# Kernel tuning notes

Measured on AMD Instinct MI355X. Metric: run time of the kernel, lower is better.

The kernel has to match this reference:

```python
import jax, jax.numpy as jnp
from jax import lax
import numpy as np

N, C, T, V, M = 128, 3, 300, 25, 2
EPS = 1e-5
FLAT = 64 * 38 * 4  # 9728, encoder flatten size


def _lrelu(x):
    return jax.nn.leaky_relu(x, 0.01)


def _bn2d(x, g, b):
    # eval-mode BatchNorm2d with running_mean=0, running_var=1 (fresh init state)
    s = g * np.float32(1.0 / np.sqrt(1.0 + EPS))
    return x * s[None, :, None, None] + b[None, :, None, None]


def _conv(x, w, b):
    # Conv2d(k=3, stride=2, pad=1)
    y = lax.conv_general_dilated(x, w, (2, 2), [(1, 1), (1, 1)],
                                 dimension_numbers=('NCHW', 'OIHW', 'NCHW'))
    return y + b[None, :, None, None]


def _convT(x, w, b, out_pad):
    # ConvTranspose2d(k=3, stride=2, pad=1, output_padding=out_pad); w is torch (Cin,Cout,kh,kw)
    wt = jnp.flip(w, (2, 3)).transpose(1, 0, 2, 3)  # (Cout, Cin, kh, kw)
    pads = [(1, 1 + out_pad[0]), (1, 1 + out_pad[1])]  # k-1-pad = 1
    y = lax.conv_general_dilated(x, wt, (1, 1), pads, lhs_dilation=(2, 2),
                                 dimension_numbers=('NCHW', 'OIHW', 'NCHW'))
    return y + b[None, :, None, None]


def setup_inputs():
    key = jax.random.key(0)
    ks = iter(jax.random.split(key, 40))

    def w(shape, fan_in):
        return jax.random.normal(next(ks), shape, jnp.float32) * np.float32(1.0 / np.sqrt(fan_in))

    inp = {}
    inp['x'] = jax.random.normal(next(ks), (N, C, T, V, M), jnp.float32)
    inp['dbn_g'] = jnp.ones((150,), jnp.float32)
    inp['dbn_b'] = jnp.zeros((150,), jnp.float32)
    inp['c1_w'] = w((16, 3, 3, 3), 27)
    inp['c1_b'] = jnp.zeros((16,), jnp.float32)
    inp['bn1_g'] = jnp.ones((16,), jnp.float32)
    inp['bn1_b'] = jnp.zeros((16,), jnp.float32)
    inp['c2_w'] = w((32, 16, 3, 3), 144)
    inp['c2_b'] = jnp.zeros((32,), jnp.float32)
    inp['bn2_g'] = jnp.ones((32,), jnp.float32)
    inp['bn2_b'] = jnp.zeros((32,), jnp.float32)
    inp['c3_w'] = w((64, 32, 3, 3), 288)
    inp['c3_b'] = jnp.zeros((64,), jnp.float32)
    inp['bn3_g'] = jnp.ones((64,), jnp.float32)
    inp['bn3_b'] = jnp.zeros((64,), jnp.float32)
    inp['fc1_w'] = w((1024, FLAT), FLAT)
    inp['fc1_b'] = jnp.zeros((1024,), jnp.float32)
    inp['fc2_w'] = w((128, 1024), 1024)
    inp['fc2_b'] = jnp.zeros((128,), jnp.float32)
    inp['fc3_w'] = w((1024, 128), 128)
    inp['fc3_b'] = jnp.zeros((1024,), jnp.float32)
    inp['fc4_w'] = w((FLAT, 1024), 1024)
    inp['fc4_b'] = jnp.zeros((FLAT,), jnp.float32)
    inp['ct1_w'] = w((64, 32, 3, 3), 576)
    inp['ct1_b'] = jnp.zeros((32,), jnp.float32)
    inp['bn4_g'] = jnp.ones((32,), jnp.float32)
    inp['bn4_b'] = jnp.zeros((32,), jnp.float32)
    inp['ct2_w'] = w((32, 16, 3, 3), 288)
    inp['ct2_b'] = jnp.zeros((16,), jnp.float32)
    inp['bn5_g'] = jnp.ones((16,), jnp.float32)
    inp['bn5_b'] = jnp.zeros((16,), jnp.float32)
    inp['ct3_w'] = w((16, 3, 3, 3), 144)
    inp['ct3_b'] = jnp.zeros((3,), jnp.float32)
    return inp


def reference(x, dbn_g, dbn_b, c1_w, c1_b, bn1_g, bn1_b, c2_w, c2_b, bn2_g, bn2_b,
              c3_w, c3_b, bn3_g, bn3_b, fc1_w, fc1_b, fc2_w, fc2_b, fc3_w, fc3_b,
              fc4_w, fc4_b, ct1_w, ct1_b, bn4_g, bn4_b, ct2_w, ct2_b, bn5_g, bn5_b,
              ct3_w, ct3_b):
    n, c, t, v, m = x.shape
    # data_bn over (N, M*V*C, T), eval-mode with running_mean=0, running_var=1
    xb = x.transpose(0, 4, 3, 1, 2).reshape(n, m * v * c, t)
    s = dbn_g * np.float32(1.0 / np.sqrt(1.0 + EPS))
    xb = xb * s[None, :, None] + dbn_b[None, :, None]
    xm = xb.reshape(n, m, v, c, t).transpose(0, 1, 3, 4, 2).reshape(n * m, c, t, v)

    dm = xm[:, :, 1:, :] - xm[:, :, :-1, :]  # (NM, C, T-1, V) frame-wise motion

    # encoder
    h = _lrelu(_bn2d(_conv(dm, c1_w, c1_b), bn1_g, bn1_b))
    h = _lrelu(_bn2d(_conv(h, c2_w, c2_b), bn2_g, bn2_b))
    h = _lrelu(_bn2d(_conv(h, c3_w, c3_b), bn3_g, bn3_b))
    h = h.reshape(n * m, -1)  # (NM, 9728)
    h = _lrelu(h @ fc1_w.T + fc1_b)
    h = _lrelu(h @ fc2_w.T + fc2_b)

    # decoder
    h = _lrelu(h @ fc3_w.T + fc3_b)
    h = _lrelu(h @ fc4_w.T + fc4_b)
    h = h.reshape(n * m, 64, 38, 4)
    h = _lrelu(_bn2d(_convT(h, ct1_w, ct1_b, (1, 1)), bn4_g, bn4_b))
    h = _lrelu(_bn2d(_convT(h, ct2_w, ct2_b, (1, 1)), bn5_g, bn5_b))
    dec = jnp.tanh(_convT(h, ct3_w, ct3_b, (0, 1)))  # (NM, 3, 303, 32)

    d = dec[:, :c, :t, :v]
    d = d.at[:, :, 0, :].set(xm[:, :, 0, :])  # seed frame 0 with input positions

    # cumulative-sum-with-reset over time: the torch double loop is a scan
    z = jnp.all(dm == 0, axis=(1, 3))                       # (NM, T-1) reset flags
    z = jnp.concatenate([z, jnp.zeros((n * m, 1), bool)], 1)  # last frame never reset
    dT = d.transpose(2, 0, 1, 3)  # (T, NM, C, V)
    zT = z.T                      # (T, NM)

    def step(carry, inp):
        dt, zt = inp
        fin = jnp.where(zt[:, None, None], jnp.float32(0.0), dt + carry)
        return fin, fin

    _, outs = lax.scan(step, jnp.zeros_like(dT[0]), (dT, zT))
    r = outs.transpose(1, 2, 0, 3)  # (NM, C, T, V)
    return r.reshape(n, m, c, t, v).transpose(0, 2, 3, 4, 1)  # (N, C, T, V, M)
```

## Files before the change

### kernel.cpp

```cpp
#include <hip/hip_runtime.h>
#include <math.h>

#define LRELU(y) ((y) > 0.f ? (y) : 0.01f * (y))
__device__ __constant__ float BNS = 0.99999500003749969f;

typedef unsigned short u16;
typedef __attribute__((ext_vector_type(8))) short bf16x8;
typedef __attribute__((ext_vector_type(4))) float f32x4;

__device__ inline u16 f2b(float f) {
  union { float f; unsigned u; } x; x.f = f;
  return (u16)((x.u + 0x7FFFu + ((x.u >> 16) & 1u)) >> 16);
}
__device__ inline float b2f(u16 b) {
  union { unsigned u; float f; } x; x.u = ((unsigned)b) << 16;
  return x.f;
}
__device__ inline float4 b2f4(ushort4 u) {
  float4 r;
  r.x = b2f(u.x); r.y = b2f(u.y); r.z = b2f(u.z); r.w = b2f(u.w);
  return r;
}
__device__ inline float ldv(const float* p) { return *p; }
__device__ inline float ldv(const u16* p) { return b2f(*p); }

__device__ inline float ftanh(float x) {
  float e = __expf(2.0f * fabsf(x));
  float t = 1.0f - 2.0f / (e + 1.0f);
  return x < 0.f ? -t : t;
}

#define FM16(I0, I1, I2, I3, WV)                                        \
  a00 += (I0) * (WV).x; a01 += (I0) * (WV).y;                           \
  a02 += (I0) * (WV).z; a03 += (I0) * (WV).w;                           \
  a10 += (I1) * (WV).x; a11 += (I1) * (WV).y;                           \
  a12 += (I1) * (WV).z; a13 += (I1) * (WV).w;                           \
  a20 += (I2) * (WV).x; a21 += (I2) * (WV).y;                           \
  a22 += (I2) * (WV).z; a23 += (I2) * (WV).w;                           \
  a30 += (I3) * (WV).x; a31 += (I3) * (WV).y;                           \
  a32 += (I3) * (WV).z; a33 += (I3) * (WV).w;

#define FM12(I0, I1, I2, I3, WV)                                        \
  a0x += (I0) * (WV).x; a0y += (I0) * (WV).y; a0z += (I0) * (WV).z;     \
  a1x += (I1) * (WV).x; a1y += (I1) * (WV).y; a1z += (I1) * (WV).z;     \
  a2x += (I2) * (WV).x; a2y += (I2) * (WV).y; a2z += (I2) * (WV).z;     \
  a3x += (I3) * (WV).x; a3y += (I3) * (WV).y; a3z += (I3) * (WV).z;

__device__ __constant__ short SCH76[4][2][3] = {
  {{3, 0, 64}, {0, 0, 64}},
  {{3, 64, 76}, {0, 64, 76}},
  {{1, 0, 64}, {2, 0, 64}},
  {{1, 64, 76}, {2, 64, 76}},
};
__device__ __constant__ short SCH152[4][3][3] = {
  {{3, 0, 64}, {1, 128, 152}, {0, 0, 64}},
  {{3, 64, 128}, {2, 0, 64}, {0, 64, 128}},
  {{3, 128, 152}, {2, 64, 128}, {0, 128, 152}},
  {{1, 0, 64}, {1, 64, 128}, {2, 128, 152}},
};

__global__ __launch_bounds__(256) void cast_kernel(
    const float* __restrict__ s, u16* __restrict__ d, int n4) {
  int i = blockIdx.x * 256 + threadIdx.x;
  if (i >= n4) return;
  float4 v = ((const float4*)s)[i];
  ushort4 o;
  o.x = f2b(v.x); o.y = f2b(v.y); o.z = f2b(v.z); o.w = f2b(v.w);
  ((ushort4*)d)[i] = o;
}

__global__ __launch_bounds__(256) void wcast_fc1_kernel(
    const float* __restrict__ w, u16* __restrict__ wp) {
  int idx = blockIdx.x * 256 + threadIdx.x;
  if (idx >= 1024 * 9728) return;
  int n = idx / 9728, kp = idx % 9728;
  int sp = kp >> 6, oc = kp & 63;
  wp[idx] = f2b(w[(long)n * 9728 + oc * 152 + sp]);
}

__global__ __launch_bounds__(256) void wpad_kernel(
    const float* __restrict__ w, u16* __restrict__ wp, int OC, int K, int KP) {
  int idx = blockIdx.x * 256 + threadIdx.x;
  if (idx >= 64 * KP) return;
  int row = idx / KP, col = idx % KP;
  wp[idx] = (row < OC && col < K) ? f2b(w[row * K + col]) : (u16)0;
}

__global__ __launch_bounds__(256) void prep_kernel(
    const float* __restrict__ x, const float* __restrict__ g,
    const float* __restrict__ b, float* __restrict__ dm,
    float* __restrict__ x0) {
  int idx = blockIdx.x * 256 + threadIdx.x;
  if (idx >= 256 * 3 * 300 * 25) return;
  int v = idx % 25;
  int t = (idx / 25) % 300;
  int c = (idx / (25 * 300)) % 3;
  int nm = idx / (25 * 300 * 3);
  int n = nm >> 1, m = nm & 1;
  int ch = m * 75 + v * 3 + c;
  float s = g[ch] * BNS, bb = b[ch];
  long xi = (((long)(n * 3 + c) * 300 + t) * 25 + v) * 2 + m;
  float xm_t = x[xi] * s + bb;
  if (t == 0) x0[(nm * 3 + c) * 25 + v] = xm_t;
  if (t < 299) {
    float xm_t1 = x[xi + 50] * s + bb;
    dm[((nm * 3 + c) * 299 + t) * 25 + v] = xm_t1 - xm_t;
  }
}

__global__ __launch_bounds__(256) void zflag_kernel(
    const float* __restrict__ dm, unsigned char* __restrict__ z) {
  int gw = blockIdx.x * 4 + (threadIdx.x >> 6);
  if (gw >= 256 * 300) return;
  int lane = threadIdx.x & 63;
  int t = gw % 300, nm = gw / 300;
  bool nz = false;
  if (t < 299) {
    const float* base = dm + (long)nm * 3 * 299 * 25 + t * 25;
    if (lane < 75) {
      int c = lane / 25, v = lane % 25;
      nz = base[c * 299 * 25 + v] != 0.f;
    }
    int l2 = lane + 64;
    if (l2 < 75) {
      int c = l2 / 25, v = l2 % 25;
      nz = nz || (base[c * 299 * 25 + v] != 0.f);
    }
  }
  unsigned long long mask = __ballot(nz);
  if (lane == 0) z[nm * 300 + t] = (unsigned char)((t < 299) && (mask == 0ull));
}

template <typename TI, int IC, int OC, int OCB, int ACC, int H, int W, int OH,
          int OW, int TOH, int NTILE>
__global__ __launch_bounds__(256) void conv_tiled_kernel(
    const TI* __restrict__ in, const float* __restrict__ w,
    const float* __restrict__ cb, const float* __restrict__ bg,
    const float* __restrict__ bnb, u16* __restrict__ out) {
  constexpr int IHT = 2 * TOH + 1;
  constexpr int RL = W + 2;
  __shared__ float in_s[IC * IHT * RL];
  __shared__ float w_s[9 * IC * OCB];
  int bx = blockIdx.x;
  int nm = blockIdx.y;
  int tile = bx % NTILE;
  int oc0 = (bx / NTILE) * OCB;
  int oh0 = tile * TOH;
  int ih0 = 2 * oh0 - 1;
  const TI* inb = in + (long)nm * IC * H * W;
  for (int e = threadIdx.x; e < IC * IHT * RL; e += 256) {
    int c = e % RL;
    int r = (e / RL) % IHT;
    int ic = e / (RL * IHT);
    int ih = ih0 + r, iw = c - 1;
    float v = 0.f;
    if (ih >= 0 && ih < H && iw >= 0 && iw < W) v = ldv(&inb[(ic * H + ih) * W + iw]);
    in_s[e] = v;
  }
  for (int e = threadIdx.x; e < 9 * IC * OCB; e += 256) {
    int ocl = e % OCB;
    int ic = (e / OCB) % IC;
    int khw = e / (OCB * IC);
    int kh = khw / 3, kw = khw % 3;
    w_s[e] = w[(((oc0 + ocl) * IC + ic) * 3 + kh) * 3 + kw];
  }
  __syncthreads();
  constexpr int NPOS = TOH * OW;
  constexpr int NWI = NPOS * (OCB / ACC);
  for (int wi = threadIdx.x; wi < NWI; wi += 256) {
    int pos = wi % NPOS;
    int jb = (wi / NPOS) * ACC;
    int ow = pos % OW;
    int oh_l = pos / OW;
    int oh = oh0 + oh_l;
    if (oh >= OH) continue;
    float acc[ACC];
#pragma unroll
    for (int j = 0; j < ACC; ++j) acc[j] = 0.f;
    for (int kh = 0; kh < 3; ++kh) {
      int r = 2 * oh_l + kh;
      for (int kw = 0; kw < 3; ++kw) {
        int cc = 2 * ow + kw;
        const float* ip = &in_s[r * RL + cc];
        const float* wp = &w_s[(kh * 3 + kw) * IC * OCB + jb];
        for (int ic = 0; ic < IC; ++ic) {
          float a = ip[ic * IHT * RL];
#pragma unroll
          for (int j = 0; j < ACC; ++j) acc[j] += a * wp[ic * OCB + j];
        }
      }
    }
#pragma unroll
    for (int j = 0; j < ACC; ++j) {
      int oc = oc0 + jb + j;
      float y = (acc[j] + cb[oc]) * (bg[oc] * BNS) + bnb[oc];
      out[((long)nm * OC + oc) * OH * OW + oh * OW + ow] = f2b(LRELU(y));
    }
  }
}

template <int IC, int H, int W, int OWW, int K, int KP, bool NHWC>
__global__ __launch_bounds__(256) void im2col_kernel(
    const u16* __restrict__ in, u16* __restrict__ patch, int m_off,
    int spatial, int n_threads) {
  int idx = blockIdx.x * 256 + threadIdx.x;
  if (idx >= n_threads) return;
  constexpr int KP8 = KP / 8;
  int m = idx / KP8;
  int k0 = (idx % KP8) * 8;
  int gm = m_off + m;
  int nm = gm / spatial, sp = gm % spatial;
  int oh = sp / OWW, ow = sp % OWW;
  __align__(16) u16 vals[8];
#pragma unroll
  for (int j = 0; j < 8; ++j) {
    int k = k0 + j;
    u16 v = 0;
    if (k < K) {
      int ic = k / 9, tap = k % 9;
      int ih = 2 * oh + tap / 3 - 1, iw = 2 * ow + tap % 3 - 1;
      if ((unsigned)ih < (unsigned)H && (unsigned)iw < (unsigned)W)
        v = NHWC ? in[((long)nm * H * W + ih * W + iw) * IC + ic]
                 : in[((long)nm * IC + ic) * H * W + ih * W + iw];
    }
    vals[j] = v;
  }
  *(uint4*)(patch + (long)m * KP + k0) = *(uint4*)vals;
}

template <int EPI>
__global__ __launch_bounds__(256) void fc_mfma_kernel(
    const u16* __restrict__ A, const u16* __restrict__ Wt,
    const float* __restrict__ p0, const float* __restrict__ p1,
    const float* __restrict__ p2, u16* __restrict__ out,
    float* __restrict__ partial, int K, int N, int ksegLen, int nvalid) {
  __shared__ u16 As[64][72];
  __shared__ u16 Bs[64][72];
  int tid = threadIdx.x;
  int m0 = blockIdx.x * 64, n0 = blockIdx.y * 64;
  long kbase = (long)blockIdx.z * ksegLen;
  int row = tid >> 3;
  int seg = (tid & 7) * 8;
  const u16* ap0 = A + (long)(m0 + row) * K + kbase + seg;
  const u16* ap1 = A + (long)(m0 + row + 32) * K + kbase + seg;
  const u16* bp0 = Wt + (long)(n0 + row) * K + kbase + seg;
  const u16* bp1 = Wt + (long)(n0 + row + 32) * K + kbase + seg;
  uint4 ra0 = *(const uint4*)ap0;
  uint4 ra1 = *(const uint4*)ap1;
  uint4 rb0 = *(const uint4*)bp0;
  uint4 rb1 = *(const uint4*)bp1;
  int wv = tid >> 6, lane = tid & 63;
  int lr = lane & 15, q = lane >> 4;
  int mb = (wv >> 1) * 32, nb = (wv & 1) * 32;
  f32x4 acc[2][2] = {};
  for (int k0 = 0; k0 < ksegLen; k0 += 64) {
    *(uint4*)&As[row][seg] = ra0;
    *(uint4*)&As[row + 32][seg] = ra1;
    *(uint4*)&Bs[row][seg] = rb0;
    *(uint4*)&Bs[row + 32][seg] = rb1;
    __syncthreads();
    if (k0 + 64 < ksegLen) {
      ra0 = *(const uint4*)(ap0 + k0 + 64);
      ra1 = *(const uint4*)(ap1 + k0 + 64);
      rb0 = *(const uint4*)(bp0 + k0 + 64);
      rb1 = *(const uint4*)(bp1 + k0 + 64);
    }
#pragma unroll
    for (int kk = 0; kk < 64; kk += 32) {
      bf16x8 a0 = *(bf16x8*)&As[mb + lr][kk + q * 8];
      bf16x8 a1 = *(bf16x8*)&As[mb + 16 + lr][kk + q * 8];
      bf16x8 b0 = *(bf16x8*)&Bs[nb + lr][kk + q * 8];
      bf16x8 b1 = *(bf16x8*)&Bs[nb + 16 + lr][kk + q * 8];
      acc[0][0] = __builtin_amdgcn_mfma_f32_16x16x32_bf16(a0, b0, acc[0][0], 0, 0, 0);
      acc[0][1] = __builtin_amdgcn_mfma_f32_16x16x32_bf16(a0, b1, acc[0][1], 0, 0, 0);
      acc[1][0] = __builtin_amdgcn_mfma_f32_16x16x32_bf16(a1, b0, acc[1][0], 0, 0, 0);
      acc[1][1] = __builtin_amdgcn_mfma_f32_16x16x32_bf16(a1, b1, acc[1][1], 0, 0, 0);
    }
    __syncthreads();
  }
#pragma unroll
  for (int mi = 0; mi < 2; ++mi)
#pragma unroll
    for (int ni = 0; ni < 2; ++ni) {
      int col = n0 + nb + ni * 16 + lr;
      if (EPI == 2 && col >= nvalid) continue;
      float b0v = 0.f, scv = 1.f, shv = 0.f;
      if (EPI == 1) b0v = p0[col];
      if (EPI == 2) { b0v = p0[col]; scv = p1[col] * BNS; shv = p2[col]; }
#pragma unroll
      for (int r = 0; r < 4; ++r) {
        int grow = m0 + mb + mi * 16 + q * 4 + r;
        float y = acc[mi][ni][r];
        if (EPI == 0) {
          partial[((long)blockIdx.z * 256 + grow) * N + col] = y;
        } else if (EPI == 1) {
          out[(long)grow * N + col] = f2b(LRELU(y + b0v));
        } else {
          out[(long)grow * N + col] = f2b(LRELU((y + b0v) * scv + shv));
        }
      }
    }
}

__global__ __launch_bounds__(256) void fc_reduce_kernel(
    const float* __restrict__ partial, const float* __restrict__ bias,
    u16* __restrict__ out, int MN, int N, int S) {
  int i = blockIdx.x * 256 + threadIdx.x;
  if (i * 4 >= MN) return;
  float4 s = ((const float4*)partial)[i];
  for (int t = 1; t < S; ++t) {
    float4 p = ((const float4*)partial)[(long)t * (MN >> 2) + i];
    s.x += p.x; s.y += p.y; s.z += p.z; s.w += p.w;
  }
  int col = (i * 4) % N;
  float4 bv = *(const float4*)(bias + col);
  ushort4 o;
  o.x = f2b(LRELU(s.x + bv.x));
  o.y = f2b(LRELU(s.y + bv.y));
  o.z = f2b(LRELU(s.z + bv.z));
  o.w = f2b(LRELU(s.w + bv.w));
  ((ushort4*)out)[i] = o;
}

template <int IC, int OCTOT, int OCB, int IH, int IW, int TOH, int NTILEH>
__global__ __launch_bounds__(256) void convt_cls_kernel(
    const u16* __restrict__ in, const float* __restrict__ w,
    const float* __restrict__ cb, const float* __restrict__ bg,
    const float* __restrict__ bnb, u16* __restrict__ out) {
  constexpr int AA = TOH / 2;
  constexpr int IHT = AA + 1;
  constexpr int RW = IW + 4;
  constexpr int OH = 2 * IH, OW = 2 * IW;
  constexpr int BG = IW / 4;
  constexpr int OG = OCB / 4;
  constexpr int CLS = AA * BG * OG;
  static_assert(CLS == 76 || CLS == 152, "schedule table missing");
  constexpr int NSEG = (CLS == 76) ? 2 : 3;
  __shared__ __align__(16) u16 in_s[IC * IHT * RW];
  __shared__ __align__(16) u16 w_s[9 * IC * OCB];
  int nm = blockIdx.y;
  int tile = blockIdx.x % NTILEH;
  int oc0 = (blockIdx.x / NTILEH) * OCB;
  int oh0 = tile * TOH;
  int ihb = oh0 >> 1;
  const u16* inb = in + (long)nm * IC * IH * IW;
  for (int e = threadIdx.x; e < IC * IHT * RW; e += 256) {
    int cw = e % RW;
    int r = (e / RW) % IHT;
    int ic = e / (RW * IHT);
    int ih = ihb + r;
    u16 v = 0;
    if (cw < IW && ih < IH) v = inb[(ic * IH + ih) * IW + cw];
    in_s[e] = v;
  }
  for (int e = threadIdx.x; e < 9 * IC * OCB; e += 256) {
    int ocl = e % OCB;
    int ic = (e / OCB) % IC;
    int khw = e / (OCB * IC);
    w_s[e] = f2b(w[(ic * OCTOT + oc0 + ocl) * 9 + khw]);
  }
  __syncthreads();
  int wvid = threadIdx.x >> 6;
  int lane = threadIdx.x & 63;
  const short(*sch)[3] = (CLS == 76) ? SCH76[wvid] : SCH152[wvid];
#pragma unroll 1
  for (int s = 0; s < NSEG; ++s) {
    int c = sch[s][0];
    int i0 = sch[s][1], i1 = sch[s][2];
    int p = c >> 1, q = c & 1;
#pragma unroll 1
    for (int rem = i0 + lane; rem < i1; rem += 64) {
      int a = rem % AA;
      int t2 = rem / AA;
      int bgi = t2 % BG;
      int og = t2 / BG;
      int b0 = bgi * 4, oc = og * 4;
      float a00 = 0.f, a01 = 0.f, a02 = 0.f, a03 = 0.f;
      float a10 = 0.f, a11 = 0.f, a12 = 0.f, a13 = 0.f;
      float a20 = 0.f, a21 = 0.f, a22 = 0.f, a23 = 0.f;
      float a30 = 0.f, a31 = 0.f, a32 = 0.f, a33 = 0.f;
#pragma unroll 1
      for (int kh = 0; kh < 3; ++kh) {
        int th = p + 1 - kh;
        if (th & 1) continue;
        int r = a + (th >> 1);
        const u16* ib = &in_s[r * RW + b0];
        const u16* wb = &w_s[(kh * 3) * IC * OCB + oc];
        if (q == 0) {
#pragma unroll 1
          for (int ic = 0; ic < IC; ++ic) {
            float4 iv = b2f4(*(const ushort4*)(ib + ic * IHT * RW));
            float4 wv1 = b2f4(*(const ushort4*)(wb + (IC + ic) * OCB));
            FM16(iv.x, iv.y, iv.z, iv.w, wv1);
          }
        } else {
#pragma unroll 1
          for (int ic = 0; ic < IC; ++ic) {
            float4 iv = b2f4(*(const ushort4*)(ib + ic * IHT * RW));
            float x4 = b2f(ib[ic * IHT * RW + 4]);
            float4 wv2 = b2f4(*(const ushort4*)(wb + (2 * IC + ic) * OCB));
            FM16(iv.x, iv.y, iv.z, iv.w, wv2);
            float4 wv0 = b2f4(*(const ushort4*)(wb + ic * OCB));
            FM16(iv.y, iv.z, iv.w, x4, wv0);
          }
        }
      }
      int oh = oh0 + 2 * a + p;
      if (oh >= OH) continue;
      int ow0 = 2 * b0 + q;
#define CT_STJ(J, A0, A1, A2, A3)                                        \
      do {                                                               \
        int o_ = oc0 + oc + (J);                                         \
        float c_ = cb[o_], s_ = bg[o_] * BNS, h_ = bnb[o_];              \
        u16* op_ = out + ((long)(nm * OCTOT + o_) * OH + oh) * OW + ow0; \
        float y0_ = ((A0) + c_) * s_ + h_;                               \
        float y1_ = ((A1) + c_) * s_ + h_;                               \
        float y2_ = ((A2) + c_) * s_ + h_;                               \
        float y3_ = ((A3) + c_) * s_ + h_;                               \
        op_[0] = f2b(LRELU(y0_)); op_[2] = f2b(LRELU(y1_));              \
        op_[4] = f2b(LRELU(y2_)); op_[6] = f2b(LRELU(y3_));              \
      } while (0)
      CT_STJ(0, a00, a10, a20, a30);
      CT_STJ(1, a01, a11, a21, a31);
      CT_STJ(2, a02, a12, a22, a32);
      CT_STJ(3, a03, a13, a23, a33);
#undef CT_STJ
    }
  }
}

__global__ __launch_bounds__(256) void convt3_cls_kernel(
    const u16* __restrict__ in, const float* __restrict__ w,
    const float* __restrict__ cb, float* __restrict__ out) {
  constexpr int IC = 16, IH = 152, IW = 16, TOH = 76;
  constexpr int AA = 38, IHT = 39, RW = 20, BG = 4;
  constexpr int CH = TOH * 25;
  __shared__ __align__(16) u16 in_s[IC * IHT * RW];
  __shared__ float w_s[9 * IC * 4];
  __shared__ __align__(16) float out_s[3 * CH];
  int nm = blockIdx.y;
  int oh0 = blockIdx.x * TOH;
  int ihb = oh0 >> 1;
  const u16* inb = in + (long)nm * IC * IH * IW;
  for (int e = threadIdx.x; e < IC * IHT * RW; e += 256) {
    int cw = e % RW;
    int r = (e / RW) % IHT;
    int ic = e / (RW * IHT);
    int ih = ihb + r;
    u16 v = 0;
    if (cw < IW && ih < IH) v = inb[(ic * IH + ih) * IW + cw];
    in_s[e] = v;
  }
  for (int e = threadIdx.x; e < 9 * IC * 4; e += 256) {
    int ocl = e % 4;
    int ic = (e / 4) % IC;
    int khw = e / 64;
    w_s[e] = (ocl < 3) ? w[(ic * 3 + ocl) * 9 + khw] : 0.f;
  }
  __syncthreads();
  float cb0 = cb[0], cb1 = cb[1], cb2 = cb[2];
  int wvid = threadIdx.x >> 6;
  int lane = threadIdx.x & 63;
  const short(*sch)[3] = SCH152[wvid];
#pragma unroll 1
  for (int s = 0; s < 3; ++s) {
    int c = sch[s][0];
    int i0 = sch[s][1], i1 = sch[s][2];
    int p = c >> 1, q = c & 1;
#pragma unroll 1
    for (int rem = i0 + lane; rem < i1; rem += 64) {
      int a = rem % AA;
      int bgi = rem / AA;
      int b0 = bgi * 4;
      float a0x = 0.f, a0y = 0.f, a0z = 0.f;
      float a1x = 0.f, a1y = 0.f, a1z = 0.f;
      float a2x = 0.f, a2y = 0.f, a2z = 0.f;
      float a3x = 0.f, a3y = 0.f, a3z = 0.f;
#pragma unroll 1
      for (int kh = 0; kh < 3; ++kh) {
        int th = p + 1 - kh;
        if (th & 1) continue;
        int r = a + (th >> 1);
        const u16* ib = &in_s[r * RW + b0];
        const float* wb = &w_s[(kh * 3) * IC * 4];
        if (q == 0) {
#pragma unroll 1
          for (int ic = 0; ic < IC; ++ic) {
            float4 iv = b2f4(*(const ushort4*)(ib + ic * IHT * RW));
            float4 wv1 = *(const float4*)(wb + (IC + ic) * 4);
            FM12(iv.x, iv.y, iv.z, iv.w, wv1);
          }
        } else {
#pragma unroll 1
          for (int ic = 0; ic < IC; ++ic) {
            float4 iv = b2f4(*(const ushort4*)(ib + ic * IHT * RW));
            float x4 = b2f(ib[ic * IHT * RW + 4]);
            float4 wv2 = *(const float4*)(wb + (2 * IC + ic) * 4);
            FM12(iv.x, iv.y, iv.z, iv.w, wv2);
            float4 wv0 = *(const float4*)(wb + ic * 4);
            FM12(iv.y, iv.z, iv.w, x4, wv0);
          }
        }
      }
      int ohl = 2 * a + p;
      int ow0 = 2 * b0 + q;
#define CT3_STB(B, AX, AY, AZ)                                           \
      do {                                                               \
        int ow_ = ow0 + 2 * (B);                                         \
        if (ow_ < 25) {                                                  \
          out_s[ohl * 25 + ow_] = (AX) + cb0;                            \
          out_s[CH + ohl * 25 + ow_] = (AY) + cb1;                       \
          out_s[2 * CH + ohl * 25 + ow_] = (AZ) + cb2;                   \
        }                                                                \
      } while (0)
      CT3_STB(0, a0x, a0y, a0z);
      CT3_STB(1, a1x, a1y, a1z);
      CT3_STB(2, a2x, a2y, a2z);
      CT3_STB(3, a3x, a3y, a3z);
#undef CT3_STB
    }
  }
  __syncthreads();
  int rows = 300 - oh0;
  if (rows > TOH) rows = TOH;
  int cnt = rows * 25;
  int tot4 = (3 * cnt) >> 2;
  for (int e4 = threadIdx.x; e4 < tot4; e4 += 256) {
    int e = e4 << 2;
    int j = e / cnt;
    int r = e - j * cnt;
    float4 v = *(const float4*)(out_s + j * CH + r);
    v.x = ftanh(v.x); v.y = ftanh(v.y); v.z = ftanh(v.z); v.w = ftanh(v.w);
    *(float4*)(out + ((long)(nm * 3 + j) * 300 + oh0) * 25 + r) = v;
  }
}

__global__ __launch_bounds__(256) void scan_kernel(
    const float* __restrict__ dec, const float* __restrict__ x0,
    const unsigned char* __restrict__ z, float* __restrict__ out) {
  int idx = blockIdx.x * 256 + threadIdx.x;
  if (idx >= 256 * 75) return;
  int v = idx % 25;
  int c = (idx / 25) % 3;
  int nm = idx / 75;
  int n = nm >> 1, m = nm & 1;
  const float* db = dec + ((long)(nm * 3 + c) * 300) * 25 + v;
  const unsigned char* zb = z + nm * 300;
  float* ob = out + (((long)(n * 3 + c) * 300) * 25 + v) * 2 + m;
  float x0v = x0[(nm * 3 + c) * 25 + v];
  float carry = 0.f;
  for (int t0 = 0; t0 < 300; t0 += 10) {
    float vals[10];
#pragma unroll
    for (int i = 0; i < 10; ++i) vals[i] = db[(t0 + i) * 25];
#pragma unroll
    for (int i = 0; i < 10; ++i) {
      int t = t0 + i;
      float d = (t == 0) ? x0v : vals[i];
      carry = zb[t] ? 0.f : (d + carry);
      ob[(long)t * 50] = carry;
    }
  }
}

extern "C" void kernel_launch(void* const* d_in, const int* in_sizes, int n_in,
                              void* d_out, int out_size, void* d_ws, size_t ws_size,
                              hipStream_t stream) {
  const float* x     = (const float*)d_in[0];
  const float* dbn_g = (const float*)d_in[1];
  const float* dbn_b = (const float*)d_in[2];
  const float* c1_w  = (const float*)d_in[3];
  const float* c1_b  = (const float*)d_in[4];
  const float* bn1_g = (const float*)d_in[5];
  const float* bn1_b = (const float*)d_in[6];
  const float* c2_w  = (const float*)d_in[7];
  const float* c2_b  = (const float*)d_in[8];
  const float* bn2_g = (const float*)d_in[9];
  const float* bn2_b = (const float*)d_in[10];
  const float* c3_w  = (const float*)d_in[11];
  const float* c3_b  = (const float*)d_in[12];
  const float* bn3_g = (const float*)d_in[13];
  const float* bn3_b = (const float*)d_in[14];
  const float* fc1_w = (const float*)d_in[15];
  const float* fc1_b = (const float*)d_in[16];
  const float* fc2_w = (const float*)d_in[17];
  const float* fc2_b = (const float*)d_in[18];
  const float* fc3_w = (const float*)d_in[19];
  const float* fc3_b = (const float*)d_in[20];
  const float* fc4_w = (const float*)d_in[21];
  const float* fc4_b = (const float*)d_in[22];
  const float* ct1_w = (const float*)d_in[23];
  const float* ct1_b = (const float*)d_in[24];
  const float* bn4_g = (const float*)d_in[25];
  const float* bn4_b = (const float*)d_in[26];
  const float* ct2_w = (const float*)d_in[27];
  const float* ct2_b = (const float*)d_in[28];
  const float* bn5_g = (const float*)d_in[29];
  const float* bn5_b = (const float*)d_in[30];
  const float* ct3_w = (const float*)d_in[31];
  const float* ct3_b = (const float*)d_in[32];
  float* out = (float*)d_out;

  char* ws = (char*)d_ws;
  unsigned char* zbuf = (unsigned char*)ws;
  float* x0 = (float*)(ws + 131072);
  char* slotA = ws + 262144;
  float* dm   = (float*)slotA;
  u16*   wbA  = (u16*)slotA;
  float* ct3o = (float*)slotA;
  char* slotB = ws + 23461888;
  u16* c1o  = (u16*)slotB;
  u16* ct2o = (u16*)slotB;
  char* slotP = ws + 44433408;
  u16*   patch   = (u16*)slotP;
  float* partial = (float*)slotP;
  u16*   ct1o    = (u16*)slotP;
  char* slotD = ws + 70254592;
  u16* c2o = (u16*)slotD;
  u16* f4  = (u16*)slotD;
  u16* c3o = (u16*)(ws + 78954496);
  u16* wb2   = (u16*)(ws + 83968000);
  u16* wb3   = (u16*)(ws + 84230144);
  u16* f1    = (u16*)(ws + 84492288);
  u16* f2    = (u16*)(ws + 85016576);
  u16* f3    = (u16*)(ws + 85082112);
  u16* w2pad = (u16*)(ws + 85606400);
  u16* w3pad = (u16*)(ws + 85630976);

  prep_kernel<<<22500, 256, 0, stream>>>(x, dbn_g, dbn_b, dm, x0);
  zflag_kernel<<<19200, 256, 0, stream>>>(dm, zbuf);

  conv_tiled_kernel<float, 3, 16, 16, 8, 299, 25, 150, 13, 30, 5>
      <<<dim3(5, 256), 256, 0, stream>>>(dm, c1_w, c1_b, bn1_g, bn1_b, c1o);

  wcast_fc1_kernel<<<38912, 256, 0, stream>>>(fc1_w, wbA);
  cast_kernel<<<128, 256, 0, stream>>>(fc2_w, wb2, 32768);
  cast_kernel<<<128, 256, 0, stream>>>(fc3_w, wb3, 32768);
  wpad_kernel<<<48, 256, 0, stream>>>(c2_w, w2pad, 32, 144, 192);
  wpad_kernel<<<80, 256, 0, stream>>>(c3_w, w3pad, 64, 288, 320);

  for (int h = 0; h < 2; ++h) {
    im2col_kernel<16, 150, 13, 7, 144, 192, false><<<6300, 256, 0, stream>>>(
        c1o, patch, h * 67200, 525, 67200 * 24);
    fc_mfma_kernel<2><<<dim3(1050, 1, 1), 256, 0, stream>>>(
        patch, w2pad, c2_b, bn2_g, bn2_b, c2o + (long)h * 67200 * 32, nullptr,
        192, 32, 192, 32);
  }
  im2col_kernel<32, 75, 7, 4, 288, 320, true><<<6080, 256, 0, stream>>>(
      c2o, patch, 0, 152, 38912 * 40);
  fc_mfma_kernel<2><<<dim3(608, 1, 1), 256, 0, stream>>>(
      patch, w3pad, c3_b, bn3_g, bn3_b, c3o, nullptr, 320, 64, 320, 64);

  fc_mfma_kernel<0><<<dim3(4, 16, 8), 256, 0, stream>>>(
      c3o, wbA, nullptr, nullptr, nullptr, nullptr, partial, 9728, 1024, 1216, 0);
  fc_reduce_kernel<<<256, 256, 0, stream>>>(partial, fc1_b, f1, 262144, 1024, 8);
  cast_kernel<<<9728, 256, 0, stream>>>(fc4_w, wbA, 2490368);
  fc_mfma_kernel<0><<<dim3(4, 2, 16), 256, 0, stream>>>(
      f1, wb2, nullptr, nullptr, nullptr, nullptr, partial, 1024, 128, 64, 0);
  fc_reduce_kernel<<<32, 256, 0, stream>>>(partial, fc2_b, f2, 32768, 128, 16);
  fc_mfma_kernel<0><<<dim3(4, 16, 2), 256, 0, stream>>>(
      f2, wb3, nullptr, nullptr, nullptr, nullptr, partial, 128, 1024, 64, 0);
  fc_reduce_kernel<<<256, 256, 0, stream>>>(partial, fc3_b, f3, 262144, 1024, 2);
  fc_mfma_kernel<1><<<dim3(4, 152, 1), 256, 0, stream>>>(
      f3, wbA, fc4_b, nullptr, nullptr, f4, nullptr, 1024, 9728, 1024, 9728);

  convt_cls_kernel<64, 32, 16, 38, 4, 38, 2>
      <<<dim3(4, 256), 256, 0, stream>>>(f4, ct1_w, ct1_b, bn4_g, bn4_b, ct1o);
  convt_cls_kernel<32, 16, 16, 76, 8, 38, 4>
      <<<dim3(4, 256), 256, 0, stream>>>(ct1o, ct2_w, ct2_b, bn5_g, bn5_b, ct2o);
  convt3_cls_kernel<<<dim3(4, 256), 256, 0, stream>>>(ct2o, ct3_w, ct3_b, ct3o);

  scan_kernel<<<75, 256, 0, stream>>>(ct3o, x0, zbuf, out);
}
```

Baseline: 618.3 us.

## Replace first transposed conv with MFMA sub-pixel GEMM kernel

The first ConvTranspose layer (64->32 channels, 38x4 -> 76x8) moves from the scalar FMA class-scheduled kernel to a new bf16 MFMA kernel. The kernel splits the work into four output parity classes, each computed as an implicit GEMM over only its contributing taps. A new prep kernel packs the ct1 weights per class into a padded bf16 layout. This targets the scalar FMA cost of ct1, at the price of an extra weight-pack launch, padding of N from 32 to 64 that wastes half the MFMA output columns, and uneven K across classes.

```diff
diff --git a/kernel.cpp b/kernel.cpp
--- a/kernel.cpp
+++ b/kernel.cpp
@@ -46,18 +46,22 @@
   a2x += (I2) * (WV).x; a2y += (I2) * (WV).y; a2z += (I2) * (WV).z;     \
   a3x += (I3) * (WV).x; a3y += (I3) * (WV).y; a3z += (I3) * (WV).z;
 
-__device__ __constant__ short SCH76[4][2][3] = {
-  {{3, 0, 64}, {0, 0, 64}},
-  {{3, 64, 76}, {0, 64, 76}},
-  {{1, 0, 64}, {2, 0, 64}},
-  {{1, 64, 76}, {2, 64, 76}},
-};
 __device__ __constant__ short SCH152[4][3][3] = {
   {{3, 0, 64}, {1, 128, 152}, {0, 0, 64}},
   {{3, 64, 128}, {2, 0, 64}, {0, 64, 128}},
   {{3, 128, 152}, {2, 64, 128}, {0, 128, 152}},
   {{1, 0, 64}, {1, 64, 128}, {2, 128, 152}},
 };
+
+__device__ __constant__ short CT1_TAPS[9][3] = {
+  {4, 0, 0},
+  {3, 0, 1}, {5, 0, 0},
+  {1, 1, 0}, {7, 0, 0},
+  {0, 1, 1}, {2, 1, 0}, {6, 0, 1}, {8, 0, 0},
+};
+__device__ __constant__ int CT1_TAPB[4] = {0, 1, 3, 5};
+__device__ __constant__ int CT1_K[4]    = {64, 128, 128, 256};
+__device__ __constant__ int CT1_CB[4]   = {0, 4096, 12288, 20480};
 
 __global__ __launch_bounds__(256) void cast_kernel(
     const float* __restrict__ s, u16* __restrict__ d, int n4) {
@@ -84,6 +88,20 @@
   if (idx >= 64 * KP) return;
   int row = idx / KP, col = idx % KP;
   wp[idx] = (row < OC && col < K) ? f2b(w[row * K + col]) : (u16)0;
+}
+
+__global__ __launch_bounds__(256) void wct1_kernel(
+    const float* __restrict__ w, u16* __restrict__ wt) {
+  int idx = blockIdx.x * 256 + threadIdx.x;
+  if (idx >= 36864) return;
+  int c = (idx < 4096) ? 0 : (idx < 12288) ? 1 : (idx < 20480) ? 2 : 3;
+  int off = idx - CT1_CB[c];
+  int K = CT1_K[c];
+  int n = off / K;
+  int rem = off - n * K;
+  int t = rem >> 6, ic = rem & 63;
+  int khw = CT1_TAPS[CT1_TAPB[c] + t][0];
+  wt[idx] = (n < 32) ? f2b(w[(ic * 32 + n) * 9 + khw]) : (u16)0;
 }
 
 __global__ __launch_bounds__(256) void prep_kernel(
@@ -322,6 +340,79 @@
   ((ushort4*)out)[i] = o;
 }
 
+__global__ __launch_bounds__(256) void ct1_mfma_kernel(
+    const u16* __restrict__ in, const u16* __restrict__ wt,
+    const float* __restrict__ cb, const float* __restrict__ bg,
+    const float* __restrict__ bnb, u16* __restrict__ out) {
+  constexpr int ICP = 72;
+  __shared__ __align__(16) u16 in_s[153 * ICP];
+  __shared__ __align__(16) u16 Bs[64][72];
+  int cls = blockIdx.x & 3, mt = blockIdx.x >> 2;
+  int nm = blockIdx.y;
+  int m0 = mt * 64;
+  int tid = threadIdx.x;
+  const u16* inb = in + (long)nm * 9728;
+  for (int e = tid; e < 9800; e += 256) {
+    if (e < 9728) in_s[(e % 152) * ICP + e / 152] = inb[e];
+    else in_s[152 * ICP + (e - 9728)] = 0;
+  }
+  int K = CT1_K[cls], cbase = CT1_CB[cls], tb = CT1_TAPB[cls];
+  int p = cls >> 1, qc = cls & 1;
+  int row = tid >> 3, seg = (tid & 7) * 8;
+  int wv = tid >> 6, lane = tid & 63;
+  int lr = lane & 15, qq = lane >> 4;
+  int mb = (wv >> 1) * 32, nb = (wv & 1) * 32;
+  f32x4 acc[2][2] = {};
+  int nstep = K >> 6;
+  for (int st = 0; st < nstep; ++st) {
+    __syncthreads();
+    *(uint4*)&Bs[row][seg] =
+        *(const uint4*)(wt + cbase + (long)row * K + st * 64 + seg);
+    *(uint4*)&Bs[row + 32][seg] =
+        *(const uint4*)(wt + cbase + (long)(row + 32) * K + st * 64 + seg);
+    __syncthreads();
+    int sh = CT1_TAPS[tb + st][1], sw = CT1_TAPS[tb + st][2];
+    int s0, s1;
+    {
+      int m = m0 + mb + lr;
+      int a = m >> 2, b = m & 3;
+      int ih = a + sh, iw = b + sw;
+      s0 = (m < 152 && ih < 38 && iw < 4) ? (ih * 4 + iw) : 152;
+      m = m0 + mb + 16 + lr;
+      a = m >> 2; b = m & 3; ih = a + sh; iw = b + sw;
+      s1 = (m < 152 && ih < 38 && iw < 4) ? (ih * 4 + iw) : 152;
+    }
+#pragma unroll
+    for (int kk = 0; kk < 64; kk += 32) {
+      bf16x8 a0 = *(bf16x8*)&in_s[s0 * ICP + kk + qq * 8];
+      bf16x8 a1 = *(bf16x8*)&in_s[s1 * ICP + kk + qq * 8];
+      bf16x8 b0 = *(bf16x8*)&Bs[nb + lr][kk + qq * 8];
+      bf16x8 b1 = *(bf16x8*)&Bs[nb + 16 + lr][kk + qq * 8];
+      acc[0][0] = __builtin_amdgcn_mfma_f32_16x16x32_bf16(a0, b0, acc[0][0], 0, 0, 0);
+      acc[0][1] = __builtin_amdgcn_mfma_f32_16x16x32_bf16(a0, b1, acc[0][1], 0, 0, 0);
+      acc[1][0] = __builtin_amdgcn_mfma_f32_16x16x32_bf16(a1, b0, acc[1][0], 0, 0, 0);
+      acc[1][1] = __builtin_amdgcn_mfma_f32_16x16x32_bf16(a1, b1, acc[1][1], 0, 0, 0);
+    }
+  }
+#pragma unroll
+  for (int mi = 0; mi < 2; ++mi)
+#pragma unroll
+    for (int ni = 0; ni < 2; ++ni) {
+      int col = nb + ni * 16 + lr;
+      if (col >= 32) continue;
+      float c_ = cb[col], s_ = bg[col] * BNS, h_ = bnb[col];
+#pragma unroll
+      for (int r = 0; r < 4; ++r) {
+        int m = m0 + mb + mi * 16 + qq * 4 + r;
+        if (m >= 152) continue;
+        int a = m >> 2, b = m & 3;
+        int oh = 2 * a + p, ow = 2 * b + qc;
+        float y = (acc[mi][ni][r] + c_) * s_ + h_;
+        out[((long)(nm * 32 + col) * 76 + oh) * 8 + ow] = f2b(LRELU(y));
+      }
+    }
+}
+
 template <int IC, int OCTOT, int OCB, int IH, int IW, int TOH, int NTILEH>
 __global__ __launch_bounds__(256) void convt_cls_kernel(
     const u16* __restrict__ in, const float* __restrict__ w,
@@ -334,8 +425,8 @@
   constexpr int BG = IW / 4;
   constexpr int OG = OCB / 4;
   constexpr int CLS = AA * BG * OG;
-  static_assert(CLS == 76 || CLS == 152, "schedule table missing");
-  constexpr int NSEG = (CLS == 76) ? 2 : 3;
+  static_assert(CLS == 152, "schedule table missing");
+  constexpr int NSEG = 3;
   __shared__ __align__(16) u16 in_s[IC * IHT * RW];
   __shared__ __align__(16) u16 w_s[9 * IC * OCB];
   int nm = blockIdx.y;
@@ -362,7 +453,7 @@
   __syncthreads();
   int wvid = threadIdx.x >> 6;
   int lane = threadIdx.x & 63;
-  const short(*sch)[3] = (CLS == 76) ? SCH76[wvid] : SCH152[wvid];
+  const short(*sch)[3] = SCH152[wvid];
 #pragma unroll 1
   for (int s = 0; s < NSEG; ++s) {
     int c = sch[s][0];
@@ -608,6 +699,7 @@
   float* dm   = (float*)slotA;
   u16*   wbA  = (u16*)slotA;
   float* ct3o = (float*)slotA;
+  u16*   wtc1 = (u16*)(ws + 20447232);
   char* slotB = ws + 23461888;
   u16* c1o  = (u16*)slotB;
   u16* ct2o = (u16*)slotB;
@@ -634,6 +726,7 @@
       <<<dim3(5, 256), 256, 0, stream>>>(dm, c1_w, c1_b, bn1_g, bn1_b, c1o);
 
   wcast_fc1_kernel<<<38912, 256, 0, stream>>>(fc1_w, wbA);
+  wct1_kernel<<<144, 256, 0, stream>>>(ct1_w, wtc1);
   cast_kernel<<<128, 256, 0, stream>>>(fc2_w, wb2, 32768);
   cast_kernel<<<128, 256, 0, stream>>>(fc3_w, wb3, 32768);
   wpad_kernel<<<48, 256, 0, stream>>>(c2_w, w2pad, 32, 144, 192);
@@ -664,8 +757,8 @@
   fc_mfma_kernel<1><<<dim3(4, 152, 1), 256, 0, stream>>>(
       f3, wbA, fc4_b, nullptr, nullptr, f4, nullptr, 1024, 9728, 1024, 9728);
 
-  convt_cls_kernel<64, 32, 16, 38, 4, 38, 2>
-      <<<dim3(4, 256), 256, 0, stream>>>(f4, ct1_w, ct1_b, bn4_g, bn4_b, ct1o);
+  ct1_mfma_kernel<<<dim3(12, 256), 256, 0, stream>>>(
+      f4, wtc1, ct1_b, bn4_g, bn4_b, ct1o);
   convt_cls_kernel<32, 16, 16, 76, 8, 38, 4>
       <<<dim3(4, 256), 256, 0, stream>>>(ct1o, ct2_w, ct2_b, bn5_g, bn5_b, ct2o);
   convt3_cls_kernel<<<dim3(4, 256), 256, 0, stream>>>(ct2o, ct3_w, ct3_b, ct3o);
```

Result: no change. 610.5 us (-1.3%).
